# Optimization experiments

Hardware: AMD Instinct MI355X
Metric: run time of the kernel (lower is better)

The kernel has to match this reference:

```python
import jax, jax.numpy as jnp
import numpy as np

N = 50000
E = 1600000
NFEAT = 256
NHID = 256
PAD_N = 60000


def setup_inputs() -> dict:
    key = jax.random.key(0)
    ks = jax.random.split(key, 8)
    x = jax.random.normal(ks[0], (N, NFEAT), dtype=jnp.float32)
    adj_rows = jax.random.randint(ks[1], (E,), 0, N)
    adj_cols = jax.random.randint(ks[2], (E,), 0, N)
    adj_vals = jax.random.uniform(ks[3], (E,), dtype=jnp.float32)
    pos_idx = jnp.arange(N)  # unique rows within padded output
    W1 = jax.random.normal(ks[4], (NFEAT, NHID), dtype=jnp.float32) * 0.05
    b1 = jax.random.normal(ks[5], (NHID,), dtype=jnp.float32) * 0.05
    W2 = jax.random.normal(ks[6], (NHID, NHID), dtype=jnp.float32) * 0.05
    b2 = jax.random.normal(ks[7], (NHID,), dtype=jnp.float32) * 0.05
    return {"x": x, "adj_rows": adj_rows, "adj_cols": adj_cols,
            "adj_vals": adj_vals, "pad_n": PAD_N, "pos_idx": pos_idx,
            "W1": W1, "b1": b1, "W2": W2, "b2": b2}


def _graph_conv(x, rows, cols, vals, W, b):
    # support = x @ W ; out = adj @ support + b  (adj in COO form)
    support = x @ W                                   # [N, H]
    msgs = vals[:, None] * support[cols]              # [E, H] gather + scale
    agg = jax.ops.segment_sum(msgs, rows, num_segments=x.shape[0])
    return agg + b


def reference(x, adj_rows, adj_cols, adj_vals, pad_n, pos_idx, W1, b1, W2, b2):
    h = jax.nn.relu(_graph_conv(x, adj_rows, adj_cols, adj_vals, W1, b1))
    # dropout: eval mode (training=False) -> identity
    h = jax.nn.relu(_graph_conv(h, adj_rows, adj_cols, adj_vals, W2, b2))
    out = jnp.zeros((pad_n, h.shape[1]), dtype=h.dtype)
    out = out.at[pos_idx].set(h)
    return out
```

## Files before the change

kernel.cpp:

```cpp
#include <hip/hip_runtime.h>
#include <hip/hip_bf16.h>

typedef __attribute__((ext_vector_type(8))) short short8;
typedef __attribute__((ext_vector_type(4))) float f32x4;
typedef __attribute__((ext_vector_type(2))) float f32x2;

#define BUK_SHIFT 7
#define BUK_ROWS 128
#define MAXBUK 400
#define NBLK_BIN 256
#define CAP2 6144

static __device__ __forceinline__ unsigned short f2bf(float f) {
    unsigned u = __float_as_uint(f);
    u += 0x7fffu + ((u >> 16) & 1u);
    return (unsigned short)(u >> 16);
}

__global__ void cvt_kernel(const float* __restrict__ in, unsigned short* __restrict__ out, int n4) {
    int i = blockIdx.x * blockDim.x + threadIdx.x;
    if (i >= n4) return;
    float4 v = reinterpret_cast<const float4*>(in)[i];
    ushort4 o;
    o.x = f2bf(v.x); o.y = f2bf(v.y); o.z = f2bf(v.z); o.w = f2bf(v.w);
    reinterpret_cast<ushort4*>(out)[i] = o;
}

__global__ void wtr_kernel(const float* __restrict__ W, unsigned short* __restrict__ Wt) {
    int k = blockIdx.x, n = threadIdx.x;
    Wt[n * 256 + k] = f2bf(W[k * 256 + n]);
}


__global__ __launch_bounds__(1024) void bin_count(const int* __restrict__ rows,
                                                  int* __restrict__ cntM, int E, int nbuk, int ce) {
    __shared__ int c[MAXBUK];
    for (int i = threadIdx.x; i < nbuk; i += 1024) c[i] = 0;
    __syncthreads();
    int s = blockIdx.x * ce, e = s + ce < E ? s + ce : E;
    for (int i = s + (int)threadIdx.x; i < e; i += 1024) atomicAdd(&c[rows[i] >> BUK_SHIFT], 1);
    __syncthreads();
    for (int i = threadIdx.x; i < nbuk; i += 1024) cntM[i * gridDim.x + blockIdx.x] = c[i];
}

__global__ __launch_bounds__(1024) void scan1_kernel(const int* __restrict__ in,
                                                     int* __restrict__ tmp,
                                                     int* __restrict__ bsum, int n) {
    __shared__ int sdata[1024];
    int i = blockIdx.x * 1024 + threadIdx.x;
    int v = (i < n) ? in[i] : 0;
    sdata[threadIdx.x] = v;
    __syncthreads();
    for (int off = 1; off < 1024; off <<= 1) {
        int t = (threadIdx.x >= (unsigned)off) ? sdata[threadIdx.x - off] : 0;
        __syncthreads();
        sdata[threadIdx.x] += t;
        __syncthreads();
    }
    if (i < n) tmp[i] = sdata[threadIdx.x] - v;
    if (threadIdx.x == 1023) bsum[blockIdx.x] = sdata[1023];
}

__global__ __launch_bounds__(512) void scan2_kernel(const int* __restrict__ bsum,
                                                    int* __restrict__ boff, int nb) {
    __shared__ int s[512];
    int t = threadIdx.x;
    int v = (t < nb) ? bsum[t] : 0;
    s[t] = v;
    __syncthreads();
    for (int off = 1; off < 512; off <<= 1) {
        int x = (t >= off) ? s[t - off] : 0;
        __syncthreads();
        s[t] += x;
        __syncthreads();
    }
    if (t < nb) boff[t] = s[t] - v;
}

__global__ void scan3_kernel(const int* __restrict__ tmp, const int* __restrict__ boff,
                             int* __restrict__ out, int n) {
    int i = blockIdx.x * blockDim.x + threadIdx.x;
    if (i < n) out[i] = tmp[i] + boff[i >> 10];
}

__global__ __launch_bounds__(1024) void bin_scatter(const int* __restrict__ rows,
                                                    const int* __restrict__ cols,
                                                    const float* __restrict__ vals,
                                                    const int* __restrict__ cntS,
                                                    unsigned int* __restrict__ cc,
                                                    unsigned char* __restrict__ rb,
                                                    int E, int nbuk, int ce) {
    __shared__ int cur[MAXBUK];
    for (int i = threadIdx.x; i < nbuk; i += 1024) cur[i] = cntS[i * gridDim.x + blockIdx.x];
    __syncthreads();
    int s = blockIdx.x * ce, e = s + ce < E ? s + ce : E;
    for (int i = s + (int)threadIdx.x; i < e; i += 1024) {
        int r = rows[i];
        int p = atomicAdd(&cur[r >> BUK_SHIFT], 1);
        cc[p] = ((unsigned)cols[i] << 16) | (unsigned)f2bf(vals[i]);
        rb[p] = (unsigned char)(r & (BUK_ROWS - 1));
    }
}

__global__ __launch_bounds__(1024) void bucket_pad(const unsigned int* __restrict__ cc,
                                                   const unsigned char* __restrict__ rb,
                                                   const int* __restrict__ cntS,
                                                   unsigned int* __restrict__ cc2,
                                                   int2* __restrict__ rp,
                                                   int E, int nbuk, int nblk, int N) {
    __shared__ int cnt[BUK_ROWS];
    __shared__ int psc[BUK_ROWS];
    __shared__ int cur[BUK_ROWS];
    const int b = blockIdx.x;
    const int tid = threadIdx.x;
    const int base = cntS[b * nblk];
    const int end = (b + 1 < nbuk) ? cntS[(b + 1) * nblk] : E;
    const int sz = end - base;
    if (tid < BUK_ROWS) cnt[tid] = 0;
    __syncthreads();
    for (int i = tid; i < sz; i += 1024) atomicAdd(&cnt[rb[base + i]], 1);
    __syncthreads();
    if (tid < BUK_ROWS) psc[tid] = (cnt[tid] + 7) & ~7;
    __syncthreads();
    for (int off = 1; off < BUK_ROWS; off <<= 1) {
        int t = (tid < BUK_ROWS && tid >= off) ? psc[tid - off] : 0;
        __syncthreads();
        if (tid < BUK_ROWS) psc[tid] += t;
        __syncthreads();
    }
    if (tid < BUK_ROWS) {
        int c = cnt[tid];
        int pc = (c + 7) & ~7;
        int excl = psc[tid] - pc;
        cur[tid] = excl;
        int st = b * CAP2 + excl;
        rp[b * BUK_ROWS + tid] = make_int2(st, st + pc);
        for (int z = c; z < pc; ++z) cc2[(size_t)st + z] = 0u;
    }
    __syncthreads();
    for (int i = tid; i < sz; i += 1024) {
        int p = atomicAdd(&cur[rb[base + i]], 1);
        cc2[(size_t)b * CAP2 + p] = cc[base + i];
    }
}

__global__ __launch_bounds__(256) void gemm_kernel(const unsigned short* __restrict__ A,
                                                   const unsigned short* __restrict__ Bt,
                                                   unsigned char* __restrict__ S8, int M) {
    __shared__ unsigned char lds[2][8192];
    const int tid = threadIdx.x;
    const int lane = tid & 63;
    const int wave = tid >> 6;
    const int m0 = blockIdx.x * 64;
    const int l15 = lane & 15;
    const int q = lane >> 4;
    const int sw = (l15 & 7) << 4;

    const int st_r0 = tid >> 3;
    const int st_c = tid & 7;
    const int st_off0 = st_r0 * 128 + ((st_c ^ (st_r0 & 7)) << 4);
    const int st_r1 = st_r0 + 32;
    const int st_off1 = st_r1 * 128 + ((st_c ^ (st_r1 & 7)) << 4);
    int row0 = m0 + st_r0; row0 = row0 < M ? row0 : 0;
    int row1 = m0 + st_r1; row1 = row1 < M ? row1 : 0;
    const unsigned short* s0p = A + (size_t)row0 * 256 + st_c * 8;
    const unsigned short* s1p = A + (size_t)row1 * 256 + st_c * 8;

    const unsigned short* bb = Bt + (size_t)(wave * 64 + l15) * 256 + q * 8;

    f32x4 acc[4][4] = {};

    uint4 s0 = *reinterpret_cast<const uint4*>(s0p);
    uint4 s1 = *reinterpret_cast<const uint4*>(s1p);
    *reinterpret_cast<uint4*>(&lds[0][st_off0]) = s0;
    *reinterpret_cast<uint4*>(&lds[0][st_off1]) = s1;
    __syncthreads();

#pragma unroll
    for (int it = 0; it < 4; ++it) {
        const int buf = it & 1;
        if (it < 3) {
            s0 = *reinterpret_cast<const uint4*>(s0p + (it + 1) * 64);
            s1 = *reinterpret_cast<const uint4*>(s1p + (it + 1) * 64);
        }
        const int kk = it * 64;
#pragma unroll
        for (int ks = 0; ks < 2; ++ks) {
            short8 a[4], b[4];
#pragma unroll
            for (int mf = 0; mf < 4; ++mf) {
                int r = mf * 16 + l15;
                a[mf] = *reinterpret_cast<const short8*>(
                    &lds[buf][r * 128 + ((ks * 64 + q * 16) ^ sw)]);
            }
#pragma unroll
            for (int nf = 0; nf < 4; ++nf)
                b[nf] = *reinterpret_cast<const short8*>(bb + (size_t)nf * 16 * 256 + kk + ks * 32);
#pragma unroll
            for (int mf = 0; mf < 4; ++mf)
#pragma unroll
                for (int nf = 0; nf < 4; ++nf)
                    acc[mf][nf] = __builtin_amdgcn_mfma_f32_16x16x32_bf16(b[nf], a[mf], acc[mf][nf], 0, 0, 0);
        }
        if (it < 3) {
            *reinterpret_cast<uint4*>(&lds[buf ^ 1][st_off0]) = s0;
            *reinterpret_cast<uint4*>(&lds[buf ^ 1][st_off1]) = s1;
        }
        __syncthreads();
    }

    const int g4 = q * 4;
#pragma unroll
    for (int mf = 0; mf < 4; ++mf) {
        int m = m0 + mf * 16 + l15;
        if (m < M) {
#pragma unroll
            for (int nf = 0; nf < 4; ++nf) {
                int p = __builtin_amdgcn_cvt_pk_fp8_f32(acc[mf][nf][0], acc[mf][nf][1], 0, false);
                p = __builtin_amdgcn_cvt_pk_fp8_f32(acc[mf][nf][2], acc[mf][nf][3], p, true);
                *reinterpret_cast<int*>(S8 + ((size_t)wave * M + m) * 64 + nf * 16 + g4) = p;
            }
        }
    }
}

template <int LAYER2>
__global__ __launch_bounds__(256) void spmm_kernel(const unsigned char* __restrict__ S8,
                                                   const int2* __restrict__ rp,
                                                   const unsigned int* __restrict__ cc,
                                                   const float* __restrict__ bias,
                                                   unsigned short* __restrict__ out_bf,
                                                   float* __restrict__ out_f,
                                                   const int* __restrict__ pos_idx, int N) {
    const int slab = blockIdx.y;
    const int lane = threadIdx.x & 63;
    const int wid = threadIdx.x >> 6;
    const int q = lane >> 4;
    const int l = lane & 15;
    const int row = blockIdx.x * 16 + wid * 4 + q;
    const int2 r = rp[row];
    float a0 = 0.f, a1 = 0.f, a2 = 0.f, a3 = 0.f;
    const unsigned char* Sl = S8 + (size_t)slab * N * 64 + l * 4;
    for (int i = r.x; i < r.y; i += 8) {
        uint4 c0 = *reinterpret_cast<const uint4*>(cc + i);
        uint4 c1 = *reinterpret_cast<const uint4*>(cc + i + 4);
        unsigned w0 = *reinterpret_cast<const unsigned*>(Sl + ((size_t)(c0.x >> 16) << 6));
        unsigned w1 = *reinterpret_cast<const unsigned*>(Sl + ((size_t)(c0.y >> 16) << 6));
        unsigned w2 = *reinterpret_cast<const unsigned*>(Sl + ((size_t)(c0.z >> 16) << 6));
        unsigned w3 = *reinterpret_cast<const unsigned*>(Sl + ((size_t)(c0.w >> 16) << 6));
        unsigned w4 = *reinterpret_cast<const unsigned*>(Sl + ((size_t)(c1.x >> 16) << 6));
        unsigned w5 = *reinterpret_cast<const unsigned*>(Sl + ((size_t)(c1.y >> 16) << 6));
        unsigned w6 = *reinterpret_cast<const unsigned*>(Sl + ((size_t)(c1.z >> 16) << 6));
        unsigned w7 = *reinterpret_cast<const unsigned*>(Sl + ((size_t)(c1.w >> 16) << 6));
        float v0 = __uint_as_float(c0.x << 16), v1 = __uint_as_float(c0.y << 16);
        float v2 = __uint_as_float(c0.z << 16), v3 = __uint_as_float(c0.w << 16);
        float v4 = __uint_as_float(c1.x << 16), v5 = __uint_as_float(c1.y << 16);
        float v6 = __uint_as_float(c1.z << 16), v7 = __uint_as_float(c1.w << 16);
#define ACC(ww, vv) { \
        f32x2 plo = __builtin_amdgcn_cvt_pk_f32_fp8((int)ww, false); \
        f32x2 phi = __builtin_amdgcn_cvt_pk_f32_fp8((int)ww, true);  \
        a0 += vv * plo.x; a1 += vv * plo.y; a2 += vv * phi.x; a3 += vv * phi.y; }
        ACC(w0, v0) ACC(w1, v1) ACC(w2, v2) ACC(w3, v3)
        ACC(w4, v4) ACC(w5, v5) ACC(w6, v6) ACC(w7, v7)
#undef ACC
    }
    if (row >= N) return;
    const int f = slab * 64 + l * 4;
    a0 = fmaxf(a0 + bias[f + 0], 0.f);
    a1 = fmaxf(a1 + bias[f + 1], 0.f);
    a2 = fmaxf(a2 + bias[f + 2], 0.f);
    a3 = fmaxf(a3 + bias[f + 3], 0.f);
    if (LAYER2) {
        int orow = pos_idx[row];
        *reinterpret_cast<float4*>(out_f + (size_t)orow * 256 + f) = make_float4(a0, a1, a2, a3);
    } else {
        ushort4 o;
        o.x = f2bf(a0); o.y = f2bf(a1); o.z = f2bf(a2); o.w = f2bf(a3);
        *reinterpret_cast<ushort4*>(out_bf + (size_t)row * 256 + f) = o;
    }
}

extern "C" void kernel_launch(void* const* d_in, const int* in_sizes, int n_in,
                              void* d_out, int out_size, void* d_ws, size_t ws_size,
                              hipStream_t stream) {
    const float* x        = (const float*)d_in[0];
    const int* adj_rows   = (const int*)d_in[1];
    const int* adj_cols   = (const int*)d_in[2];
    const float* adj_vals = (const float*)d_in[3];
    const int* pos_idx    = (const int*)d_in[5];
    const float* W1       = (const float*)d_in[6];
    const float* b1       = (const float*)d_in[7];
    const float* W2       = (const float*)d_in[8];
    const float* b2       = (const float*)d_in[9];

    const int N = in_sizes[0] / 256;
    const int E = in_sizes[1];
    const int nbuk = (N + BUK_ROWS - 1) >> BUK_SHIFT;
    const int n2 = nbuk * NBLK_BIN;
    const int nb2 = (n2 + 1023) / 1024;
    const int ce = (E + NBLK_BIN - 1) / NBLK_BIN;
    const int nwork = nbuk * BUK_ROWS;

    char* ws = (char*)d_ws;
    size_t off = 0;
    auto alloc = [&](size_t bytes) {
        char* p = ws + off;
        off += (bytes + 255) & ~(size_t)255;
        return p;
    };
    unsigned short* xb   = (unsigned short*)alloc((size_t)N * 256 * 2);
    unsigned char*  sup8 = (unsigned char*)alloc((size_t)N * 256);
    unsigned short* w1t  = (unsigned short*)alloc(256 * 256 * 2);
    unsigned short* w2t  = (unsigned short*)alloc(256 * 256 * 2);
    int2* rp     = (int2*)alloc((size_t)nwork * 8);
    int* cntM    = (int*)alloc((size_t)n2 * 4);
    int* cntS    = (int*)alloc((size_t)n2 * 4);
    int* tmp     = (int*)alloc((size_t)n2 * 4);
    int* bsum    = (int*)alloc(512 * 4);
    int* boff    = (int*)alloc(512 * 4);
    unsigned int* cc  = (unsigned int*)alloc((size_t)E * 4);
    unsigned char* rb = (unsigned char*)alloc((size_t)E);
    unsigned int* cc2 = (unsigned int*)alloc((size_t)nbuk * CAP2 * 4);
    (void)ws_size; (void)n_in;

    hipMemsetAsync((float*)d_out + (size_t)N * 256, 0,
                   ((size_t)out_size - (size_t)N * 256) * 4, stream);

    cvt_kernel<<<(N * 64 + 255) / 256, 256, 0, stream>>>(x, xb, N * 64);
    wtr_kernel<<<256, 256, 0, stream>>>(W1, w1t);
    wtr_kernel<<<256, 256, 0, stream>>>(W2, w2t);

    bin_count<<<NBLK_BIN, 1024, 0, stream>>>(adj_rows, cntM, E, nbuk, ce);
    scan1_kernel<<<nb2, 1024, 0, stream>>>(cntM, tmp, bsum, n2);
    scan2_kernel<<<1, 512, 0, stream>>>(bsum, boff, nb2);
    scan3_kernel<<<(n2 + 255) / 256, 256, 0, stream>>>(tmp, boff, cntS, n2);
    bin_scatter<<<NBLK_BIN, 1024, 0, stream>>>(adj_rows, adj_cols, adj_vals, cntS, cc, rb, E, nbuk, ce);
    bucket_pad<<<nbuk, 1024, 0, stream>>>(cc, rb, cntS, cc2, rp, E, nbuk, NBLK_BIN, N);

    const int ggrid = (N + 63) / 64;
    const dim3 sgrid(nwork / 16, 4);
    gemm_kernel<<<ggrid, 256, 0, stream>>>(xb, w1t, sup8, N);
    spmm_kernel<0><<<sgrid, 256, 0, stream>>>(sup8, rp, cc2, b1, xb, nullptr, nullptr, N);
    gemm_kernel<<<ggrid, 256, 0, stream>>>(xb, w2t, sup8, N);
    spmm_kernel<1><<<sgrid, 256, 0, stream>>>(sup8, rp, cc2, b2, nullptr, (float*)d_out, pos_idx, N);
}
```

Baseline: 231.1 us.

## Fuse fp32-to-bf16 conversion into first GEMM and stage bin scatter in LDS

Removes the separate cvt_kernel by having the first GEMM load fp32 x directly and pack it to bf16 while staging A tiles. The COO bin scatter now sorts each chunk of edges locally in shared memory by bucket, then writes contiguous runs per bucket to global memory instead of doing scattered per-edge writes. The chunk count now comes from a fixed chunk size rather than a fixed block count. The SpMM accumulation is also rewritten with packed f32x2 vector FMAs. The first GEMM reads twice the bytes for its A operand, and the scatter kernel gains a local count and scan pass plus a large LDS footprint.

```diff
diff --git a/kernel.cpp b/kernel.cpp
--- a/kernel.cpp
+++ b/kernel.cpp
@@ -8,22 +8,17 @@
 #define BUK_SHIFT 7
 #define BUK_ROWS 128
 #define MAXBUK 400
-#define NBLK_BIN 256
 #define CAP2 6144
+#define CHUNK 6250
+#define CHUNK_PAD 6272
 
 static __device__ __forceinline__ unsigned short f2bf(float f) {
     unsigned u = __float_as_uint(f);
     u += 0x7fffu + ((u >> 16) & 1u);
     return (unsigned short)(u >> 16);
 }
-
-__global__ void cvt_kernel(const float* __restrict__ in, unsigned short* __restrict__ out, int n4) {
-    int i = blockIdx.x * blockDim.x + threadIdx.x;
-    if (i >= n4) return;
-    float4 v = reinterpret_cast<const float4*>(in)[i];
-    ushort4 o;
-    o.x = f2bf(v.x); o.y = f2bf(v.y); o.z = f2bf(v.z); o.w = f2bf(v.w);
-    reinterpret_cast<ushort4*>(out)[i] = o;
+static __device__ __forceinline__ unsigned pk2bf(float a, float b) {
+    return (unsigned)f2bf(a) | ((unsigned)f2bf(b) << 16);
 }
 
 __global__ void wtr_kernel(const float* __restrict__ W, unsigned short* __restrict__ Wt) {
@@ -33,11 +28,11 @@
 
 
 __global__ __launch_bounds__(1024) void bin_count(const int* __restrict__ rows,
-                                                  int* __restrict__ cntM, int E, int nbuk, int ce) {
+                                                  int* __restrict__ cntM, int E, int nbuk) {
     __shared__ int c[MAXBUK];
     for (int i = threadIdx.x; i < nbuk; i += 1024) c[i] = 0;
     __syncthreads();
-    int s = blockIdx.x * ce, e = s + ce < E ? s + ce : E;
+    int s = blockIdx.x * CHUNK, e = s + CHUNK < E ? s + CHUNK : E;
     for (int i = s + (int)threadIdx.x; i < e; i += 1024) atomicAdd(&c[rows[i] >> BUK_SHIFT], 1);
     __syncthreads();
     for (int i = threadIdx.x; i < nbuk; i += 1024) cntM[i * gridDim.x + blockIdx.x] = c[i];
@@ -89,16 +84,42 @@
                                                     const int* __restrict__ cntS,
                                                     unsigned int* __restrict__ cc,
                                                     unsigned char* __restrict__ rb,
-                                                    int E, int nbuk, int ce) {
-    __shared__ int cur[MAXBUK];
-    for (int i = threadIdx.x; i < nbuk; i += 1024) cur[i] = cntS[i * gridDim.x + blockIdx.x];
-    __syncthreads();
-    int s = blockIdx.x * ce, e = s + ce < E ? s + ce : E;
-    for (int i = s + (int)threadIdx.x; i < e; i += 1024) {
+                                                    int E, int nbuk, int nblk) {
+    __shared__ unsigned int scc[CHUNK_PAD];
+    __shared__ unsigned char srb[CHUNK_PAD];
+    __shared__ int lcnt[512], lsc[512], lcur[512];
+    const int b = blockIdx.x, tid = threadIdx.x;
+    const int s = b * CHUNK, e = s + CHUNK < E ? s + CHUNK : E;
+    if (tid < 512) lcnt[tid] = 0;
+    __syncthreads();
+    for (int i = s + tid; i < e; i += 1024) atomicAdd(&lcnt[rows[i] >> BUK_SHIFT], 1);
+    __syncthreads();
+    if (tid < 512) lsc[tid] = lcnt[tid];
+    __syncthreads();
+    for (int off = 1; off < 512; off <<= 1) {
+        int t = (tid < 512 && tid >= off) ? lsc[tid - off] : 0;
+        __syncthreads();
+        if (tid < 512) lsc[tid] += t;
+        __syncthreads();
+    }
+    if (tid < 512) lcur[tid] = lsc[tid] - lcnt[tid];
+    __syncthreads();
+    for (int i = s + tid; i < e; i += 1024) {
         int r = rows[i];
-        int p = atomicAdd(&cur[r >> BUK_SHIFT], 1);
-        cc[p] = ((unsigned)cols[i] << 16) | (unsigned)f2bf(vals[i]);
-        rb[p] = (unsigned char)(r & (BUK_ROWS - 1));
+        int p = atomicAdd(&lcur[r >> BUK_SHIFT], 1);
+        scc[p] = ((unsigned)cols[i] << 16) | (unsigned)f2bf(vals[i]);
+        srb[p] = (unsigned char)(r & (BUK_ROWS - 1));
+    }
+    __syncthreads();
+    const int wv = tid >> 6, ln = tid & 63;
+    for (int bu = wv; bu < nbuk; bu += 16) {
+        const int lo = lsc[bu] - lcnt[bu];
+        const int n = lcnt[bu];
+        const int gbase = cntS[bu * nblk + b];
+        for (int j = ln; j < n; j += 64) {
+            cc[gbase + j] = scc[lo + j];
+            rb[gbase + j] = srb[lo + j];
+        }
     }
 }
 
@@ -144,10 +165,26 @@
     }
 }
 
-__global__ __launch_bounds__(256) void gemm_kernel(const unsigned short* __restrict__ A,
+template <int AF32>
+static __device__ __forceinline__ uint4 load_frag(const char* p) {
+    if (AF32) {
+        const float* f = (const float*)p;
+        float4 f0 = *reinterpret_cast<const float4*>(f);
+        float4 f1 = *reinterpret_cast<const float4*>(f + 4);
+        uint4 u;
+        u.x = pk2bf(f0.x, f0.y); u.y = pk2bf(f0.z, f0.w);
+        u.z = pk2bf(f1.x, f1.y); u.w = pk2bf(f1.z, f1.w);
+        return u;
+    }
+    return *reinterpret_cast<const uint4*>(p);
+}
+
+template <int AF32>
+__global__ __launch_bounds__(256) void gemm_kernel(const void* __restrict__ Av,
                                                    const unsigned short* __restrict__ Bt,
                                                    unsigned char* __restrict__ S8, int M) {
     __shared__ unsigned char lds[2][8192];
+    const int esz = AF32 ? 4 : 2;
     const int tid = threadIdx.x;
     const int lane = tid & 63;
     const int wave = tid >> 6;
@@ -163,15 +200,15 @@
     const int st_off1 = st_r1 * 128 + ((st_c ^ (st_r1 & 7)) << 4);
     int row0 = m0 + st_r0; row0 = row0 < M ? row0 : 0;
     int row1 = m0 + st_r1; row1 = row1 < M ? row1 : 0;
-    const unsigned short* s0p = A + (size_t)row0 * 256 + st_c * 8;
-    const unsigned short* s1p = A + (size_t)row1 * 256 + st_c * 8;
+    const char* s0p = (const char*)Av + ((size_t)row0 * 256 + st_c * 8) * esz;
+    const char* s1p = (const char*)Av + ((size_t)row1 * 256 + st_c * 8) * esz;
 
     const unsigned short* bb = Bt + (size_t)(wave * 64 + l15) * 256 + q * 8;
 
     f32x4 acc[4][4] = {};
 
-    uint4 s0 = *reinterpret_cast<const uint4*>(s0p);
-    uint4 s1 = *reinterpret_cast<const uint4*>(s1p);
+    uint4 s0 = load_frag<AF32>(s0p);
+    uint4 s1 = load_frag<AF32>(s1p);
     *reinterpret_cast<uint4*>(&lds[0][st_off0]) = s0;
     *reinterpret_cast<uint4*>(&lds[0][st_off1]) = s1;
     __syncthreads();
@@ -180,8 +217,8 @@
     for (int it = 0; it < 4; ++it) {
         const int buf = it & 1;
         if (it < 3) {
-            s0 = *reinterpret_cast<const uint4*>(s0p + (it + 1) * 64);
-            s1 = *reinterpret_cast<const uint4*>(s1p + (it + 1) * 64);
+            s0 = load_frag<AF32>(s0p + (size_t)(it + 1) * 64 * esz);
+            s1 = load_frag<AF32>(s1p + (size_t)(it + 1) * 64 * esz);
         }
         const int kk = it * 64;
 #pragma unroll
@@ -239,7 +276,7 @@
     const int l = lane & 15;
     const int row = blockIdx.x * 16 + wid * 4 + q;
     const int2 r = rp[row];
-    float a0 = 0.f, a1 = 0.f, a2 = 0.f, a3 = 0.f;
+    f32x2 a01 = {0.f, 0.f}, a23 = {0.f, 0.f};
     const unsigned char* Sl = S8 + (size_t)slab * N * 64 + l * 4;
     for (int i = r.x; i < r.y; i += 8) {
         uint4 c0 = *reinterpret_cast<const uint4*>(cc + i);
@@ -259,17 +296,18 @@
 #define ACC(ww, vv) { \
         f32x2 plo = __builtin_amdgcn_cvt_pk_f32_fp8((int)ww, false); \
         f32x2 phi = __builtin_amdgcn_cvt_pk_f32_fp8((int)ww, true);  \
-        a0 += vv * plo.x; a1 += vv * plo.y; a2 += vv * phi.x; a3 += vv * phi.y; }
+        f32x2 vv2 = {vv, vv}; \
+        a01 += vv2 * plo; a23 += vv2 * phi; }
         ACC(w0, v0) ACC(w1, v1) ACC(w2, v2) ACC(w3, v3)
         ACC(w4, v4) ACC(w5, v5) ACC(w6, v6) ACC(w7, v7)
 #undef ACC
     }
     if (row >= N) return;
     const int f = slab * 64 + l * 4;
-    a0 = fmaxf(a0 + bias[f + 0], 0.f);
-    a1 = fmaxf(a1 + bias[f + 1], 0.f);
-    a2 = fmaxf(a2 + bias[f + 2], 0.f);
-    a3 = fmaxf(a3 + bias[f + 3], 0.f);
+    float a0 = fmaxf(a01.x + bias[f + 0], 0.f);
+    float a1 = fmaxf(a01.y + bias[f + 1], 0.f);
+    float a2 = fmaxf(a23.x + bias[f + 2], 0.f);
+    float a3 = fmaxf(a23.y + bias[f + 3], 0.f);
     if (LAYER2) {
         int orow = pos_idx[row];
         *reinterpret_cast<float4*>(out_f + (size_t)orow * 256 + f) = make_float4(a0, a1, a2, a3);
@@ -296,9 +334,9 @@
     const int N = in_sizes[0] / 256;
     const int E = in_sizes[1];
     const int nbuk = (N + BUK_ROWS - 1) >> BUK_SHIFT;
-    const int n2 = nbuk * NBLK_BIN;
+    const int nblk = (E + CHUNK - 1) / CHUNK;
+    const int n2 = nbuk * nblk;
     const int nb2 = (n2 + 1023) / 1024;
-    const int ce = (E + NBLK_BIN - 1) / NBLK_BIN;
     const int nwork = nbuk * BUK_ROWS;
 
     char* ws = (char*)d_ws;
@@ -326,21 +364,20 @@
     hipMemsetAsync((float*)d_out + (size_t)N * 256, 0,
                    ((size_t)out_size - (size_t)N * 256) * 4, stream);
 
-    cvt_kernel<<<(N * 64 + 255) / 256, 256, 0, stream>>>(x, xb, N * 64);
     wtr_kernel<<<256, 256, 0, stream>>>(W1, w1t);
     wtr_kernel<<<256, 256, 0, stream>>>(W2, w2t);
 
-    bin_count<<<NBLK_BIN, 1024, 0, stream>>>(adj_rows, cntM, E, nbuk, ce);
+    bin_count<<<nblk, 1024, 0, stream>>>(adj_rows, cntM, E, nbuk);
     scan1_kernel<<<nb2, 1024, 0, stream>>>(cntM, tmp, bsum, n2);
     scan2_kernel<<<1, 512, 0, stream>>>(bsum, boff, nb2);
     scan3_kernel<<<(n2 + 255) / 256, 256, 0, stream>>>(tmp, boff, cntS, n2);
-    bin_scatter<<<NBLK_BIN, 1024, 0, stream>>>(adj_rows, adj_cols, adj_vals, cntS, cc, rb, E, nbuk, ce);
-    bucket_pad<<<nbuk, 1024, 0, stream>>>(cc, rb, cntS, cc2, rp, E, nbuk, NBLK_BIN, N);
+    bin_scatter<<<nblk, 1024, 0, stream>>>(adj_rows, adj_cols, adj_vals, cntS, cc, rb, E, nbuk, nblk);
+    bucket_pad<<<nbuk, 1024, 0, stream>>>(cc, rb, cntS, cc2, rp, E, nbuk, nblk, N);
 
     const int ggrid = (N + 63) / 64;
     const dim3 sgrid(nwork / 16, 4);
-    gemm_kernel<<<ggrid, 256, 0, stream>>>(xb, w1t, sup8, N);
+    gemm_kernel<1><<<ggrid, 256, 0, stream>>>(x, w1t, sup8, N);
     spmm_kernel<0><<<sgrid, 256, 0, stream>>>(sup8, rp, cc2, b1, xb, nullptr, nullptr, N);
-    gemm_kernel<<<ggrid, 256, 0, stream>>>(xb, w2t, sup8, N);
+    gemm_kernel<0><<<ggrid, 256, 0, stream>>>(xb, w2t, sup8, N);
     spmm_kernel<1><<<sgrid, 256, 0, stream>>>(sup8, rp, cc2, b2, nullptr, (float*)d_out, pos_idx, N);
 }
```

Result: faster. 224.8 us (-2.7%).
